# Kernel tuning notes

Hardware: AMD Instinct MI355X
Metric: run time of the kernel (lower is better)

Reference implementation:

```python
import jax, jax.numpy as jnp
import numpy as np

I, H, O, T = 512, 2048, 128, 4096

def setup_inputs() -> dict:
    key = jax.random.key(0)
    ks = jax.random.split(key, 7)
    s_ih = 1.0 / np.sqrt(H)
    inp = {
        "input": jax.random.normal(ks[0], (1, T, I), dtype=jnp.float32),
        # PyTorch LSTM params, gate order (i, f, g, o)
        "W_ih": jax.random.uniform(ks[1], (4 * H, I), jnp.float32, -s_ih, s_ih),
        "W_hh": jax.random.uniform(ks[2], (4 * H, H), jnp.float32, -s_ih, s_ih),
        "b_ih": jax.random.uniform(ks[3], (4 * H,), jnp.float32, -s_ih, s_ih),
        "b_hh": jax.random.uniform(ks[4], (4 * H,), jnp.float32, -s_ih, s_ih),
        "W_d": jax.random.uniform(ks[5], (O, H), jnp.float32, -s_ih, s_ih),
        "b_d": jax.random.uniform(ks[6], (O,), jnp.float32, -s_ih, s_ih),
    }
    return inp

def _lstm_dense(x, W_ih, W_hh, b_ih, b_hh, W_d, b_d):
    # x: [1, T, I], batch fixed at 1 (as in the original module)
    xs = x[0]  # [T, I]
    # precompute input-side gate contributions for all timesteps: [T, 4H]
    gx = xs @ W_ih.T + (b_ih + b_hh)
    h0 = jnp.zeros((H,), x.dtype)
    c0 = jnp.zeros((H,), x.dtype)

    def step(carry, gx_t):
        h, c = carry
        gates = gx_t + W_hh @ h  # [4H]
        i_g = jax.nn.sigmoid(gates[0 * H:1 * H])
        f_g = jax.nn.sigmoid(gates[1 * H:2 * H])
        g_g = jnp.tanh(gates[2 * H:3 * H])
        o_g = jax.nn.sigmoid(gates[3 * H:4 * H])
        c_new = f_g * c + i_g * g_g
        h_new = o_g * jnp.tanh(c_new)
        return (h_new, c_new), h_new

    _, hs = jax.lax.scan(step, (h0, c0), gx)  # hs: [T, H]
    out = hs @ W_d.T + b_d  # [T, O]
    return out[None]  # [1, T, O]

def reference(input, W_ih, W_hh, b_ih, b_hh, W_d, b_d):
    return _lstm_dense(input, W_ih, W_hh, b_ih, b_hh, W_d, b_d)
```

## Files before the change

### kernel.cpp

```cpp
#include <hip/hip_runtime.h>
#include <hip/hip_bf16.h>

#define T_STEPS 4096
#define I_DIM   512
#define H_DIM   2048
#define O_DIM   128
#define NBLK    256
#define THREADS 512
#define WAVES_PER_BLK 8
#define SENTINEL 2.0f

#define PIN2(v) asm volatile("" : "+v"((v).x), "+v"((v).y))

__global__ void fill_sentinel(float4* __restrict__ p)
{
    p[(size_t)blockIdx.x * blockDim.x + threadIdx.x] =
        make_float4(SENTINEL, SENTINEL, SENTINEL, SENTINEL);
}

__global__ __launch_bounds__(THREADS, 2)
void lstm_persistent(const float* __restrict__ x,
                     const float* __restrict__ W_ih,
                     const float* __restrict__ W_hh,
                     const float* __restrict__ b_ih,
                     const float* __restrict__ b_hh,
                     float* __restrict__ hbuf)
{
    const int tid  = threadIdx.x;
    const int wave = tid >> 6;
    const int lane = tid & 63;
    const int j    = blockIdx.x * WAVES_PER_BLK + wave;

    float2 wh2[4][16];
    float2 wx2[4][4];
    float  bs[4];
    #pragma unroll
    for (int g = 0; g < 4; ++g) {
        const int row = g * H_DIM + j;
        const float2* wp = reinterpret_cast<const float2*>(
            W_hh + (size_t)row * H_DIM + lane * 32);
        #pragma unroll
        for (int c = 0; c < 16; ++c) wh2[g][c] = wp[c];
        const float2* xp = reinterpret_cast<const float2*>(
            W_ih + (size_t)row * I_DIM + lane * 8);
        #pragma unroll
        for (int c = 0; c < 4; ++c) wx2[g][c] = xp[c];
        bs[g] = b_ih[row] + b_hh[row];
    }
    #pragma unroll
    for (int g = 0; g < 4; ++g) {
        #pragma unroll
        for (int c = 0; c < 16; ++c) PIN2(wh2[g][c]);
        #pragma unroll
        for (int c = 0; c < 4; ++c)  PIN2(wx2[g][c]);
    }

    __shared__ float hstage[64 * 34];
    __shared__ float xlds[2][64 * 10];

    xlds[0][10 * (tid >> 3) + (tid & 7)] = x[tid];
    __syncthreads();

    float c = 0.0f;

    for (int t = 0; t < T_STEPS; ++t) {
        const int cur = t & 1;

        float hv0 = 0.f, hv1 = 0.f, hv2 = 0.f, hv3 = 0.f;
        const float* hp = hbuf + (size_t)(t - 1) * H_DIM + tid;
        if (t > 0) {
            hv0 = __hip_atomic_load(hp + 0 * THREADS, __ATOMIC_RELAXED,
                                    __HIP_MEMORY_SCOPE_AGENT);
            hv1 = __hip_atomic_load(hp + 1 * THREADS, __ATOMIC_RELAXED,
                                    __HIP_MEMORY_SCOPE_AGENT);
            hv2 = __hip_atomic_load(hp + 2 * THREADS, __ATOMIC_RELAXED,
                                    __HIP_MEMORY_SCOPE_AGENT);
            hv3 = __hip_atomic_load(hp + 3 * THREADS, __ATOMIC_RELAXED,
                                    __HIP_MEMORY_SCOPE_AGENT);
        }

        if (t + 1 < T_STEPS) {
            xlds[cur ^ 1][10 * (tid >> 3) + (tid & 7)] =
                x[(size_t)(t + 1) * I_DIM + tid];
        }

        float a0 = 0.f, a1 = 0.f, a2 = 0.f, a3 = 0.f;
        {
            const float* xb = &xlds[cur][0];
            #pragma unroll
            for (int cc = 0; cc < 4; ++cc) {
                const float2 xv =
                    *reinterpret_cast<const float2*>(xb + 10 * lane + 2 * cc);
                a0 = fmaf(wx2[0][cc].x, xv.x, fmaf(wx2[0][cc].y, xv.y, a0));
                a1 = fmaf(wx2[1][cc].x, xv.x, fmaf(wx2[1][cc].y, xv.y, a1));
                a2 = fmaf(wx2[2][cc].x, xv.x, fmaf(wx2[2][cc].y, xv.y, a2));
                a3 = fmaf(wx2[3][cc].x, xv.x, fmaf(wx2[3][cc].y, xv.y, a3));
            }
        }

        if (t > 0) {
            while (hv0 == SENTINEL || hv1 == SENTINEL ||
                   hv2 == SENTINEL || hv3 == SENTINEL) {
                __builtin_amdgcn_s_sleep(1);
                hv0 = __hip_atomic_load(hp + 0 * THREADS, __ATOMIC_RELAXED,
                                        __HIP_MEMORY_SCOPE_AGENT);
                hv1 = __hip_atomic_load(hp + 1 * THREADS, __ATOMIC_RELAXED,
                                        __HIP_MEMORY_SCOPE_AGENT);
                hv2 = __hip_atomic_load(hp + 2 * THREADS, __ATOMIC_RELAXED,
                                        __HIP_MEMORY_SCOPE_AGENT);
                hv3 = __hip_atomic_load(hp + 3 * THREADS, __ATOMIC_RELAXED,
                                        __HIP_MEMORY_SCOPE_AGENT);
            }
            hstage[34 * ((tid + 0 * THREADS) >> 5) + ((tid + 0 * THREADS) & 31)] = hv0;
            hstage[34 * ((tid + 1 * THREADS) >> 5) + ((tid + 1 * THREADS) & 31)] = hv1;
            hstage[34 * ((tid + 2 * THREADS) >> 5) + ((tid + 2 * THREADS) & 31)] = hv2;
            hstage[34 * ((tid + 3 * THREADS) >> 5) + ((tid + 3 * THREADS) & 31)] = hv3;
        }
        __syncthreads();

        if (t > 0) {
            const float* hb = hstage + 34 * lane;
            #pragma unroll
            for (int cc = 0; cc < 16; ++cc) {
                const float2 hv =
                    *reinterpret_cast<const float2*>(hb + 2 * cc);
                a0 = fmaf(wh2[0][cc].x, hv.x, fmaf(wh2[0][cc].y, hv.y, a0));
                a1 = fmaf(wh2[1][cc].x, hv.x, fmaf(wh2[1][cc].y, hv.y, a1));
                a2 = fmaf(wh2[2][cc].x, hv.x, fmaf(wh2[2][cc].y, hv.y, a2));
                a3 = fmaf(wh2[3][cc].x, hv.x, fmaf(wh2[3][cc].y, hv.y, a3));
            }
        }

        #pragma unroll
        for (int m = 1; m < 64; m <<= 1) {
            a0 += __shfl_xor(a0, m, 64);
            a1 += __shfl_xor(a1, m, 64);
            a2 += __shfl_xor(a2, m, 64);
            a3 += __shfl_xor(a3, m, 64);
        }

        const float si = 1.0f / (1.0f + __expf(-(a0 + bs[0])));
        const float sf = 1.0f / (1.0f + __expf(-(a1 + bs[1])));
        const float gt = 1.0f - 2.0f / (1.0f + __expf(2.0f * (a2 + bs[2])));
        const float so = 1.0f / (1.0f + __expf(-(a3 + bs[3])));

        c = fmaf(sf, c, si * gt);
        const float tc = 1.0f - 2.0f / (1.0f + __expf(2.0f * c));
        const float h_new = so * tc;

        if (lane == 0) {
            __hip_atomic_store(hbuf + (size_t)t * H_DIM + j, h_new,
                               __ATOMIC_RELAXED, __HIP_MEMORY_SCOPE_AGENT);
        }
        __syncthreads();
    }
}

__global__ void transpose_wd(const float* __restrict__ W_d,
                             float* __restrict__ WdT)
{
    const int idx = blockIdx.x * blockDim.x + threadIdx.x;
    const int o = idx & (O_DIM - 1);
    const int k = idx >> 7;
    if (k < H_DIM) WdT[(size_t)k * O_DIM + o] = W_d[(size_t)o * H_DIM + k];
}

#define TB 8
__global__ __launch_bounds__(256)
void dense_out(const float* __restrict__ hbuf, const float* __restrict__ WdT,
               const float* __restrict__ b_d, float* __restrict__ out)
{
    __shared__ float hs[TB][H_DIM];
    const int t0 = blockIdx.x * TB;

    for (int i = threadIdx.x; i < TB * H_DIM / 4; i += 256) {
        reinterpret_cast<float4*>(&hs[0][0])[i] =
            reinterpret_cast<const float4*>(hbuf + (size_t)t0 * H_DIM)[i];
    }
    __syncthreads();

    const int o  = threadIdx.x & (O_DIM - 1);
    const int th = threadIdx.x >> 7;
    float a0 = b_d[o], a1 = a0, a2 = a0, a3 = a0;
    for (int k = 0; k < H_DIM; ++k) {
        const float w = WdT[(size_t)k * O_DIM + o];
        a0 = fmaf(hs[th * 4 + 0][k], w, a0);
        a1 = fmaf(hs[th * 4 + 1][k], w, a1);
        a2 = fmaf(hs[th * 4 + 2][k], w, a2);
        a3 = fmaf(hs[th * 4 + 3][k], w, a3);
    }
    out[(size_t)(t0 + th * 4 + 0) * O_DIM + o] = a0;
    out[(size_t)(t0 + th * 4 + 1) * O_DIM + o] = a1;
    out[(size_t)(t0 + th * 4 + 2) * O_DIM + o] = a2;
    out[(size_t)(t0 + th * 4 + 3) * O_DIM + o] = a3;
}

extern "C" void kernel_launch(void* const* d_in, const int* in_sizes, int n_in,
                              void* d_out, int out_size, void* d_ws, size_t ws_size,
                              hipStream_t stream)
{
    (void)in_sizes; (void)n_in; (void)out_size; (void)ws_size;
    const float* x    = (const float*)d_in[0];
    const float* W_ih = (const float*)d_in[1];
    const float* W_hh = (const float*)d_in[2];
    const float* b_ih = (const float*)d_in[3];
    const float* b_hh = (const float*)d_in[4];
    const float* W_d  = (const float*)d_in[5];
    const float* b_d  = (const float*)d_in[6];
    float* out = (float*)d_out;

    char* ws = (char*)d_ws;
    float* hbuf = (float*)ws;
    float* WdT  = (float*)(ws + (size_t)T_STEPS * H_DIM * 4);

    fill_sentinel<<<(T_STEPS * H_DIM / 4) / 256, 256, 0, stream>>>(
        (float4*)hbuf);
    transpose_wd<<<(H_DIM * O_DIM) / 256, 256, 0, stream>>>(W_d, WdT);
    lstm_persistent<<<NBLK, THREADS, 0, stream>>>(x, W_ih, W_hh, b_ih, b_hh,
                                                  hbuf);
    dense_out<<<T_STEPS / TB, 256, 0, stream>>>(hbuf, WdT, b_d, out);
}
```

Baseline: 14.44 ms.

## Split LSTM gate rows across wave pairs and double persistent block count

Each hidden unit's four gate rows are now split across two waves, each holding two rows of W_hh/W_ih in registers, instead of one wave holding all four. The block count doubles to 512 with 4 units per block, and pre-activations are exchanged through shared memory plus an extra __syncthreads per step. This halves per-wave register pressure and FMA work per step, and spreads the recurrent work over more CUs and waves. In exchange it adds an extra block barrier every step and doubles the number of blocks polling the global h buffer. All 512 blocks must be co-resident or the spin-wait deadlocks.

```diff
diff --git a/kernel.cpp b/kernel.cpp
--- a/kernel.cpp
+++ b/kernel.cpp
@@ -5,9 +5,8 @@
 #define I_DIM   512
 #define H_DIM   2048
 #define O_DIM   128
-#define NBLK    256
+#define NBLK    512
 #define THREADS 512
-#define WAVES_PER_BLK 8
 #define SENTINEL 2.0f
 
 #define PIN2(v) asm volatile("" : "+v"((v).x), "+v"((v).y))
@@ -18,7 +17,7 @@
         make_float4(SENTINEL, SENTINEL, SENTINEL, SENTINEL);
 }
 
-__global__ __launch_bounds__(THREADS, 2)
+__global__ __launch_bounds__(THREADS, 4)
 void lstm_persistent(const float* __restrict__ x,
                      const float* __restrict__ W_ih,
                      const float* __restrict__ W_hh,
@@ -29,34 +28,42 @@
     const int tid  = threadIdx.x;
     const int wave = tid >> 6;
     const int lane = tid & 63;
-    const int j    = blockIdx.x * WAVES_PER_BLK + wave;
-
-    float2 wh2[4][16];
-    float2 wx2[4][4];
-    float  bs[4];
+    const int u    = wave >> 1;
+    const int p    = wave & 1;
+    const int j    = blockIdx.x * 4 + u;
+
+    float2 wh2[2][16];
+    float2 wx2[2][4];
+    float  bs0, bs1;
+    {
+        const int r0 = (2 * p + 0) * H_DIM + j;
+        const int r1 = (2 * p + 1) * H_DIM + j;
+        const float2* wp0 = reinterpret_cast<const float2*>(
+            W_hh + (size_t)r0 * H_DIM + lane * 32);
+        const float2* wp1 = reinterpret_cast<const float2*>(
+            W_hh + (size_t)r1 * H_DIM + lane * 32);
+        #pragma unroll
+        for (int c = 0; c < 16; ++c) { wh2[0][c] = wp0[c]; wh2[1][c] = wp1[c]; }
+        const float2* xp0 = reinterpret_cast<const float2*>(
+            W_ih + (size_t)r0 * I_DIM + lane * 8);
+        const float2* xp1 = reinterpret_cast<const float2*>(
+            W_ih + (size_t)r1 * I_DIM + lane * 8);
+        #pragma unroll
+        for (int c = 0; c < 4; ++c) { wx2[0][c] = xp0[c]; wx2[1][c] = xp1[c]; }
+        bs0 = b_ih[r0] + b_hh[r0];
+        bs1 = b_ih[r1] + b_hh[r1];
+    }
     #pragma unroll
-    for (int g = 0; g < 4; ++g) {
-        const int row = g * H_DIM + j;
-        const float2* wp = reinterpret_cast<const float2*>(
-            W_hh + (size_t)row * H_DIM + lane * 32);
-        #pragma unroll
-        for (int c = 0; c < 16; ++c) wh2[g][c] = wp[c];
-        const float2* xp = reinterpret_cast<const float2*>(
-            W_ih + (size_t)row * I_DIM + lane * 8);
-        #pragma unroll
-        for (int c = 0; c < 4; ++c) wx2[g][c] = xp[c];
-        bs[g] = b_ih[row] + b_hh[row];
-    }
-    #pragma unroll
-    for (int g = 0; g < 4; ++g) {
-        #pragma unroll
-        for (int c = 0; c < 16; ++c) PIN2(wh2[g][c]);
-        #pragma unroll
-        for (int c = 0; c < 4; ++c)  PIN2(wx2[g][c]);
+    for (int q = 0; q < 2; ++q) {
+        #pragma unroll
+        for (int c = 0; c < 16; ++c) PIN2(wh2[q][c]);
+        #pragma unroll
+        for (int c = 0; c < 4; ++c)  PIN2(wx2[q][c]);
     }
 
     __shared__ float hstage[64 * 34];
     __shared__ float xlds[2][64 * 10];
+    __shared__ float gsum[4][2];
 
     xlds[0][10 * (tid >> 3) + (tid & 7)] = x[tid];
     __syncthreads();
@@ -84,7 +91,7 @@
                 x[(size_t)(t + 1) * I_DIM + tid];
         }
 
-        float a0 = 0.f, a1 = 0.f, a2 = 0.f, a3 = 0.f;
+        float a0 = 0.f, a1 = 0.f;
         {
             const float* xb = &xlds[cur][0];
             #pragma unroll
@@ -93,8 +100,6 @@
                     *reinterpret_cast<const float2*>(xb + 10 * lane + 2 * cc);
                 a0 = fmaf(wx2[0][cc].x, xv.x, fmaf(wx2[0][cc].y, xv.y, a0));
                 a1 = fmaf(wx2[1][cc].x, xv.x, fmaf(wx2[1][cc].y, xv.y, a1));
-                a2 = fmaf(wx2[2][cc].x, xv.x, fmaf(wx2[2][cc].y, xv.y, a2));
-                a3 = fmaf(wx2[3][cc].x, xv.x, fmaf(wx2[3][cc].y, xv.y, a3));
             }
         }
 
@@ -126,8 +131,6 @@
                     *reinterpret_cast<const float2*>(hb + 2 * cc);
                 a0 = fmaf(wh2[0][cc].x, hv.x, fmaf(wh2[0][cc].y, hv.y, a0));
                 a1 = fmaf(wh2[1][cc].x, hv.x, fmaf(wh2[1][cc].y, hv.y, a1));
-                a2 = fmaf(wh2[2][cc].x, hv.x, fmaf(wh2[2][cc].y, hv.y, a2));
-                a3 = fmaf(wh2[3][cc].x, hv.x, fmaf(wh2[3][cc].y, hv.y, a3));
             }
         }
 
@@ -135,22 +138,32 @@
         for (int m = 1; m < 64; m <<= 1) {
             a0 += __shfl_xor(a0, m, 64);
             a1 += __shfl_xor(a1, m, 64);
-            a2 += __shfl_xor(a2, m, 64);
-            a3 += __shfl_xor(a3, m, 64);
-        }
-
-        const float si = 1.0f / (1.0f + __expf(-(a0 + bs[0])));
-        const float sf = 1.0f / (1.0f + __expf(-(a1 + bs[1])));
-        const float gt = 1.0f - 2.0f / (1.0f + __expf(2.0f * (a2 + bs[2])));
-        const float so = 1.0f / (1.0f + __expf(-(a3 + bs[3])));
-
-        c = fmaf(sf, c, si * gt);
-        const float tc = 1.0f - 2.0f / (1.0f + __expf(2.0f * c));
-        const float h_new = so * tc;
-
-        if (lane == 0) {
-            __hip_atomic_store(hbuf + (size_t)t * H_DIM + j, h_new,
-                               __ATOMIC_RELAXED, __HIP_MEMORY_SCOPE_AGENT);
+        }
+        const float pre0 = a0 + bs0;
+        const float pre1 = a1 + bs1;
+
+        if (p == 0 && lane == 0) {
+            gsum[u][0] = pre0;
+            gsum[u][1] = pre1;
+        }
+        __syncthreads();
+
+        if (p == 1) {
+            const float pi = gsum[u][0];
+            const float pf = gsum[u][1];
+            const float si = 1.0f / (1.0f + __expf(-pi));
+            const float sf = 1.0f / (1.0f + __expf(-pf));
+            const float gt = 1.0f - 2.0f / (1.0f + __expf(2.0f * pre0));
+            const float so = 1.0f / (1.0f + __expf(-pre1));
+
+            c = fmaf(sf, c, si * gt);
+            const float tc = 1.0f - 2.0f / (1.0f + __expf(2.0f * c));
+            const float h_new = so * tc;
+
+            if (lane == 0) {
+                __hip_atomic_store(hbuf + (size_t)t * H_DIM + j, h_new,
+                                   __ATOMIC_RELAXED, __HIP_MEMORY_SCOPE_AGENT);
+            }
         }
         __syncthreads();
     }
```

Measured after the change: 25.03 ms. 73.4% more time.
